# Kernel tuning notes

Measured on AMD Instinct MI355X. Metric: run time of the kernel, lower is better.

The kernel has to match this reference:

```python
import jax, jax.numpy as jnp
import numpy as np

DIM = 256; QK = 256; HEADS = 8; TOPK = 2; WV = 2; WH = 2
SCALE = QK ** -0.5


def setup_inputs() -> dict:
    key = jax.random.key(0)
    ks = jax.random.split(key, 6)
    x = jax.random.normal(ks[0], (4, DIM, 64, 64), jnp.float32)
    Wqkv = jax.random.normal(ks[1], (DIM, 2 * QK + DIM), jnp.float32) * 0.02
    bqkv = jnp.zeros((2 * QK + DIM,), jnp.float32)
    Wo = jax.random.normal(ks[2], (DIM, DIM), jnp.float32) * 0.02
    bo = jnp.zeros((DIM,), jnp.float32)
    lepe_w = jax.random.normal(ks[3], (3, 3, 1, DIM), jnp.float32) * 0.1  # HWIO depthwise
    lepe_b = jnp.zeros((DIM,), jnp.float32)
    return {"x": x, "Wqkv": Wqkv, "bqkv": bqkv, "Wo": Wo, "bo": bo,
            "lepe_w": lepe_w, "lepe_b": lepe_b}


def _dwconv(x, w, b):
    # depthwise 3x3 conv, NHWC
    y = jax.lax.conv_general_dilated(x, w, (1, 1), 'SAME',
                                     dimension_numbers=('NHWC', 'HWIO', 'NHWC'),
                                     feature_group_count=x.shape[-1])
    return y + b


def _branch(win, Wqkv, bqkv, lepe_w, lepe_b, to_image):
    n, p2, h, w, _ = win.shape
    w2 = h * w
    qkv = win @ Wqkv + bqkv
    q = qkv[..., :QK]
    kv = qkv[..., QK:]                                  # [n,p2,h,w,QK+DIM]
    q_pix = q.reshape(n, p2, w2, QK)
    kv_pix = kv.reshape(n, p2, w2, QK + DIM)            # identity kv_down
    # region routing (detached in original)
    q_win = jax.lax.stop_gradient(q).mean((2, 3))       # [n,p2,QK]
    k_win = jax.lax.stop_gradient(kv[..., :QK]).mean((2, 3))
    logit = jnp.einsum('npc,nqc->npq', q_win * SCALE, k_win)
    _, r_idx = jax.lax.top_k(logit, TOPK)               # [n,p2,TOPK]
    # gather selected KV windows (mul_weight='none')
    kv_sel = jax.vmap(lambda kvb, idxb: kvb[idxb])(kv_pix, r_idx)  # [n,p2,k,w2,ckv]
    k_sel = kv_sel[..., :QK].reshape(n, p2, TOPK * w2, HEADS, QK // HEADS)
    v_sel = kv_sel[..., QK:].reshape(n, p2, TOPK * w2, HEADS, DIM // HEADS)
    qh = q_pix.reshape(n, p2, w2, HEADS, QK // HEADS)
    attn = jax.nn.softmax(jnp.einsum('npqhd,npkhd->nphqk', qh * SCALE, k_sel), axis=-1)
    out = jnp.einsum('nphqk,npkhd->npqhd', attn, v_sel).reshape(n, p2, h, w, DIM)
    lepe = _dwconv(to_image(kv[..., QK:]), lepe_w, lepe_b)
    return to_image(out) + lepe


def reference(x, Wqkv, bqkv, Wo, bo, lepe_w, lepe_b):
    xh = x.transpose(0, 2, 3, 1)                        # NHWC
    N, H, W, C = xh.shape
    v_win, h_win = H // WV, W // WH
    # vertical branch: horizontal strips of height WV, full width
    vm = xh.reshape(N, v_win, WV, W, C)
    # horizontal branch: vertical strips of width WH, full height
    hm = xh.reshape(N, H, h_win, WH, C).transpose(0, 2, 1, 3, 4)
    img_v = lambda a: a.reshape(N, H, W, a.shape[-1])
    img_h = lambda a: a.transpose(0, 2, 1, 3, 4).reshape(N, H, W, a.shape[-1])
    o1 = _branch(vm, Wqkv, bqkv, lepe_w, lepe_b, img_v)
    o2 = _branch(hm, Wqkv, bqkv, lepe_w, lepe_b, img_h)
    out = (o1 @ Wo + bo) + (o2 @ Wo + bo)
    return out.transpose(0, 3, 1, 2)                    # back to NCHW
```

## Files before the change

kernel.cpp:

```cpp
#include <hip/hip_runtime.h>
#include <hip/hip_bf16.h>
#include <math.h>

#define NBATCH 4
#define HW     4096
#define NPIX   16384
#define SCALE  0.0625f
#define QLOG2E (0.0625f * 1.44269504088896340736f)

typedef __attribute__((ext_vector_type(8))) short bf16x8;
typedef __attribute__((ext_vector_type(4))) float f32x4;

__device__ __forceinline__ int pixmap(int b, int n, int p, int pos){
  return (b == 0) ? (n*HW + p*128 + pos)
                  : (n*HW + (pos >> 1)*64 + (p << 1) + (pos & 1));
}

__device__ __forceinline__ ushort f2b(float x){
  __hip_bfloat16 h = __float2bfloat16(x);
  return *reinterpret_cast<ushort*>(&h);
}
__device__ __forceinline__ float b2f(ushort u){
  __hip_bfloat16 h = *reinterpret_cast<__hip_bfloat16*>(&u);
  return __bfloat162float(h);
}
__device__ __forceinline__ uint pk2(float a, float b){
  return (uint)f2b(a) | ((uint)f2b(b) << 16);
}

__global__ __launch_bounds__(256) void k_xt(
    const float* __restrict__ x, ushort* __restrict__ Xb)
{
  __shared__ float T[32][257];
  const int n = blockIdx.y, hw0 = blockIdx.x * 32;
  const int tid = threadIdx.x;
  const int hl = tid & 31, cg = tid >> 5;
  #pragma unroll 8
  for(int i = 0; i < 32; i++){
    const int c = i*8 + cg;
    T[hl][c] = x[((size_t)(n*256 + c))*4096 + hw0 + hl];
  }
  __syncthreads();
  const int c0 = (tid & 31)*8, pb = tid >> 5;
  #pragma unroll
  for(int i = 0; i < 4; i++){
    const int p = pb + 8*i;
    union { bf16x8 v; ushort u[8]; } U;
    #pragma unroll
    for(int j = 0; j < 8; j++) U.u[j] = f2b(T[p][c0 + j]);
    *(bf16x8*)(Xb + ((size_t)(n*HW + hw0 + p))*256 + c0) = U.v;
  }
}

__global__ __launch_bounds__(256) void k_wt(
    const float* __restrict__ Wqkv, ushort* __restrict__ Wt)
{
  const int o = blockIdx.x, t = threadIdx.x;
  Wt[(size_t)o*256 + t] = f2b(Wqkv[(size_t)t*768 + o]);
}

__global__ __launch_bounds__(256) void k_wto(
    const float* __restrict__ Wo, ushort* __restrict__ WoT)
{
  const int o = blockIdx.x, t = threadIdx.x;
  WoT[(size_t)o*256 + t] = f2b(Wo[(size_t)t*256 + o]);
}

__global__ __launch_bounds__(256) void k_qkv_mfma(
    const ushort* __restrict__ Xb, const ushort* __restrict__ Wt,
    const float* __restrict__ bqkv, ushort* __restrict__ QKVb,
    ushort* __restrict__ Vt)
{
  const int tid = threadIdx.x;
  const int l = tid & 63, w = tid >> 6;
  const int wr = w >> 1, wc = w & 1;
  const int q16 = l & 15, g = l >> 4;
  const int row0 = blockIdx.x*128 + wr*64;
  const int col0 = blockIdx.y*128 + wc*64;

  f32x4 acc[4][4];
  #pragma unroll
  for(int i = 0; i < 4; i++)
    #pragma unroll
    for(int j = 0; j < 4; j++) acc[i][j] = (f32x4){0,0,0,0};

  const ushort* Ab = Xb + (size_t)(row0 + q16)*256 + 8*g;
  const ushort* Bb = Wt + (size_t)(col0 + q16)*256 + 8*g;

  #pragma unroll
  for(int ks = 0; ks < 8; ks++){
    const int k0 = ks*32;
    bf16x8 a[4], b[4];
    #pragma unroll
    for(int i = 0; i < 4; i++) a[i] = *(const bf16x8*)(Ab + (size_t)(16*i)*256 + k0);
    #pragma unroll
    for(int j = 0; j < 4; j++) b[j] = *(const bf16x8*)(Bb + (size_t)(16*j)*256 + k0);
    #pragma unroll
    for(int i = 0; i < 4; i++)
      #pragma unroll
      for(int j = 0; j < 4; j++)
        acc[i][j] = __builtin_amdgcn_mfma_f32_16x16x32_bf16(a[i], b[j], acc[i][j], 0, 0, 0);
  }

  const int n = row0 >> 12, hwb = row0 & 4095;
  #pragma unroll
  for(int j = 0; j < 4; j++){
    const int col = col0 + 16*j + q16;
    const float bias = bqkv[col];
    const float sc = (col < 256) ? QLOG2E : 1.f;
    #pragma unroll
    for(int i = 0; i < 4; i++){
      ushort4 u;
      u.x = f2b((acc[i][j][0] + bias) * sc);
      u.y = f2b((acc[i][j][1] + bias) * sc);
      u.z = f2b((acc[i][j][2] + bias) * sc);
      u.w = f2b((acc[i][j][3] + bias) * sc);
      const int row = row0 + 16*i + 4*g;
      QKVb[(size_t)(row+0)*768 + col] = u.x;
      QKVb[(size_t)(row+1)*768 + col] = u.y;
      QKVb[(size_t)(row+2)*768 + col] = u.z;
      QKVb[(size_t)(row+3)*768 + col] = u.w;
      if(col >= 512){
        *(ushort4*)&Vt[((size_t)(n*256 + col - 512))*4096 + hwb + 16*i + 4*g] = u;
      }
    }
  }
}

__global__ __launch_bounds__(256) void k_xmean(
    const float* __restrict__ x, float* __restrict__ xwin)
{
  const int n = blockIdx.y;
  const int c = blockIdx.x*4 + (threadIdx.x >> 6);
  const int l = threadIdx.x & 63;
  const float* xc = x + ((size_t)(n*256 + c))*4096;

  float4 cs[8];
  #pragma unroll
  for(int i = 0; i < 8; i++) cs[i] = (float4){0,0,0,0};
  float rsum = 0.f;
  const float4* xr = (const float4*)(xc + l*64);
  #pragma unroll
  for(int i = 0; i < 16; i++){
    const float4 v = xr[i];
    rsum += (v.x+v.y)+(v.z+v.w);
    const float p0 = v.x+v.y, p1 = v.z+v.w;
    if(i & 1){ cs[i>>1].z += p0; cs[i>>1].w += p1; }
    else     { cs[i>>1].x += p0; cs[i>>1].y += p1; }
  }
  #pragma unroll
  for(int i = 0; i < 8; i++){
    #pragma unroll
    for(int s = 1; s < 64; s <<= 1){
      cs[i].x += __shfl_xor(cs[i].x, s);
      cs[i].y += __shfl_xor(cs[i].y, s);
      cs[i].z += __shfl_xor(cs[i].z, s);
      cs[i].w += __shfl_xor(cs[i].w, s);
    }
  }
  const int p = l & 31;
  const float rp = __shfl(rsum, 2*p) + __shfl(rsum, 2*p + 1);
  float cp;
  {
    const int hi = p >> 2, lo = p & 3;
    const float4 q = hi==0?cs[0]:hi==1?cs[1]:hi==2?cs[2]:hi==3?cs[3]
                   : hi==4?cs[4]:hi==5?cs[5]:hi==6?cs[6]:cs[7];
    cp = lo==0?q.x : lo==1?q.y : lo==2?q.z : q.w;
  }
  if(l < 32){
    xwin[((size_t)((0*NBATCH + n)*32 + p))*256 + c] = rp * (1.f/128.f);
    xwin[((size_t)((1*NBATCH + n)*32 + p))*256 + c] = cp * (1.f/128.f);
  }
}

__global__ __launch_bounds__(256) void k_win_gemm(
    const float* __restrict__ xwin, const float* __restrict__ Wqkv,
    const float* __restrict__ bqkv, float* __restrict__ qwin, float* __restrict__ kwin)
{
  __shared__ float xs[256];
  const int row = blockIdx.x;
  const int tid = threadIdx.x;
  xs[tid] = xwin[(size_t)row*256 + tid];
  __syncthreads();
  #pragma unroll
  for(int half = 0; half < 2; half++){
    const int col = half*256 + tid;
    float s = 0.f;
    for(int k = 0; k < 256; k++) s += xs[k] * Wqkv[(size_t)k*768 + col];
    s += bqkv[col];
    if(half == 0) qwin[(size_t)row*256 + tid] = s;
    else          kwin[(size_t)row*256 + tid] = s;
  }
}

__global__ __launch_bounds__(256) void k_logits_top2(
    const float* __restrict__ qwin, const float* __restrict__ kwin, int* __restrict__ ridx)
{
  const int n = blockIdx.x, b = blockIdx.y;
  __shared__ float lg[32][32];
  const int base = ((b*NBATCH + n)*32)*256;
  for(int t = threadIdx.x; t < 1024; t += 256){
    const int p = t >> 5, q = t & 31;
    const float* qp = qwin + base + p*256;
    const float* kq = kwin + base + q*256;
    float s = 0.f;
    for(int c = 0; c < 256; c++) s += qp[c]*kq[c];
    lg[p][q] = s * SCALE;
  }
  __syncthreads();
  if(threadIdx.x < 32){
    const int p = threadIdx.x;
    float m0 = -INFINITY; int i0 = 0;
    for(int q = 0; q < 32; q++){ const float v = lg[p][q]; if(v > m0){ m0 = v; i0 = q; } }
    float m1 = -INFINITY; int i1 = 0;
    for(int q = 0; q < 32; q++){ if(q == i0) continue; const float v = lg[p][q]; if(v > m1){ m1 = v; i1 = q; } }
    const int o = ((b*NBATCH + n)*32 + p)*2;
    ridx[o] = i0; ridx[o+1] = i1;
  }
}

__global__ __launch_bounds__(256) void k_attn_mfma(
    const ushort* __restrict__ QKVb, const ushort* __restrict__ Vt,
    const int* __restrict__ ridx, ushort* __restrict__ Ob)
{
  int id = blockIdx.x*4 + (threadIdx.x >> 6);
  const int half = id & 1; id >>= 1;
  const int hd = id & 7;  id >>= 3;
  const int p  = id & 31; id >>= 5;
  const int n  = id & 3;  id >>= 2;
  const int b  = id;
  const int l = threadIdx.x & 63;
  const int q16 = l & 15, g = l >> 4;

  const int ro = ((b*NBATCH + n)*32 + p)*2;
  const int r0 = ridx[ro], r1 = ridx[ro+1];

  int qpix[4];
  bf16x8 qf[4];
  #pragma unroll
  for(int m = 0; m < 4; m++){
    qpix[m] = pixmap(b, n, p, (half*4 + m)*16 + q16);
    qf[m] = *(const bf16x8*)(QKVb + (size_t)qpix[m]*768 + hd*32 + 8*g);
  }

  f32x4 acc0[4], acc1[4];
  float rs[4];
  #pragma unroll
  for(int m = 0; m < 4; m++){
    acc0[m] = (f32x4){0,0,0,0}; acc1[m] = (f32x4){0,0,0,0}; rs[m] = 0.f;
  }

  for(int c = 0; c < 8; c++){
    const int wsel = (c < 4) ? r0 : r1;
    const int posb = (32*c) & 127;

    bf16x8 kf0, kf1;
    {
      const int kp0 = pixmap(b, n, wsel, posb + q16);
      kf0 = *(const bf16x8*)(QKVb + (size_t)kp0*768 + 256 + hd*32 + 8*g);
      const int kp1 = pixmap(b, n, wsel, posb + 16 + q16);
      kf1 = *(const bf16x8*)(QKVb + (size_t)kp1*768 + 256 + hd*32 + 8*g);
    }
    bf16x8 vf0, vf1;
    if(b == 0){
      const ushort* base = Vt + ((size_t)(n*256 + hd*32 + q16))*4096 + wsel*128 + posb + 4*g;
      union { bf16x8 v; ushort4 h[2]; } U0, U1;
      U0.h[0] = *(const ushort4*)(base);
      U0.h[1] = *(const ushort4*)(base + 16);
      U1.h[0] = *(const ushort4*)(base + (size_t)16*4096);
      U1.h[1] = *(const ushort4*)(base + (size_t)16*4096 + 16);
      vf0 = U0.v; vf1 = U1.v;
    } else {
      const int h0 = (posb + 4*g) >> 1;
      const ushort* base = Vt + ((size_t)(n*256 + hd*32 + q16))*4096 + 2*wsel;
      union { bf16x8 v; uint u[4]; } U0, U1;
      U0.u[0] = *(const uint*)(base + (h0    )*64);
      U0.u[1] = *(const uint*)(base + (h0 + 1)*64);
      U0.u[2] = *(const uint*)(base + (h0 + 8)*64);
      U0.u[3] = *(const uint*)(base + (h0 + 9)*64);
      const ushort* base1 = base + (size_t)16*4096;
      U1.u[0] = *(const uint*)(base1 + (h0    )*64);
      U1.u[1] = *(const uint*)(base1 + (h0 + 1)*64);
      U1.u[2] = *(const uint*)(base1 + (h0 + 8)*64);
      U1.u[3] = *(const uint*)(base1 + (h0 + 9)*64);
      vf0 = U0.v; vf1 = U1.v;
    }

    #pragma unroll
    for(int m = 0; m < 4; m++){
      const f32x4 z = {0,0,0,0};
      f32x4 s0 = __builtin_amdgcn_mfma_f32_16x16x32_bf16(kf0, qf[m], z, 0, 0, 0);
      f32x4 s1 = __builtin_amdgcn_mfma_f32_16x16x32_bf16(kf1, qf[m], z, 0, 0, 0);
      const float e00 = exp2f(s0[0]), e01 = exp2f(s0[1]), e02 = exp2f(s0[2]), e03 = exp2f(s0[3]);
      const float e10 = exp2f(s1[0]), e11 = exp2f(s1[1]), e12 = exp2f(s1[2]), e13 = exp2f(s1[3]);
      rs[m] += ((e00+e01)+(e02+e03)) + ((e10+e11)+(e12+e13));
      union { bf16x8 v; uint u[4]; } P;
      P.u[0] = pk2(e00, e01);
      P.u[1] = pk2(e02, e03);
      P.u[2] = pk2(e10, e11);
      P.u[3] = pk2(e12, e13);
      acc0[m] = __builtin_amdgcn_mfma_f32_16x16x32_bf16(vf0, P.v, acc0[m], 0, 0, 0);
      acc1[m] = __builtin_amdgcn_mfma_f32_16x16x32_bf16(vf1, P.v, acc1[m], 0, 0, 0);
    }
  }

  #pragma unroll
  for(int m = 0; m < 4; m++){
    float r = rs[m];
    r += __shfl_xor(r, 16);
    r += __shfl_xor(r, 32);
    rs[m] = 1.f / r;
  }
  #pragma unroll
  for(int m = 0; m < 4; m++){
    ushort* op = Ob + ((size_t)b*NPIX + qpix[m])*256 + hd*32 + 4*g;
    const float iv = rs[m];
    ushort4 o0 = { f2b(acc0[m][0]*iv), f2b(acc0[m][1]*iv), f2b(acc0[m][2]*iv), f2b(acc0[m][3]*iv) };
    ushort4 o1 = { f2b(acc1[m][0]*iv), f2b(acc1[m][1]*iv), f2b(acc1[m][2]*iv), f2b(acc1[m][3]*iv) };
    *(ushort4*)op = o0;
    *(ushort4*)(op + 16) = o1;
  }
}

__global__ __launch_bounds__(256) void k_combine_lepe(
    const ushort* __restrict__ QKVb, const ushort* __restrict__ Ob0,
    const ushort* __restrict__ Ob1,
    const float* __restrict__ lw, const float* __restrict__ lb, ushort* __restrict__ Sb)
{
  const int pix = blockIdx.x;
  const int c = threadIdx.x;
  const int n = pix >> 12, rem = pix & 4095;
  const int h = rem >> 6, w = rem & 63;
  float conv = 0.f;
  #pragma unroll
  for(int kh = 0; kh < 3; kh++){
    const int hh = h + kh - 1;
    if(hh < 0 || hh >= 64) continue;
    #pragma unroll
    for(int kw = 0; kw < 3; kw++){
      const int wi = w + kw - 1;
      if(wi < 0 || wi >= 64) continue;
      const int np = (n*64 + hh)*64 + wi;
      conv += b2f(QKVb[(size_t)np*768 + 512 + c]) * lw[(kh*3 + kw)*256 + c];
    }
  }
  const size_t idx = (size_t)pix*256 + c;
  Sb[idx] = f2b(b2f(Ob0[idx]) + b2f(Ob1[idx]) + 2.f*(conv + lb[c]));
}

__global__ __launch_bounds__(256) void k_out_mfma(
    const ushort* __restrict__ Sb, const ushort* __restrict__ WoT,
    const float* __restrict__ bo, float* __restrict__ out)
{
  const int tid = threadIdx.x;
  const int l = tid & 63, w = tid >> 6;
  const int wr = w >> 1, wc = w & 1;
  const int q16 = l & 15, g = l >> 4;
  const int c0   = blockIdx.x*128 + wr*64;
  const int pix0 = blockIdx.y*128 + wc*64;
  const int n = pix0 >> 12, rem0 = pix0 & 4095;

  f32x4 acc[4][4];
  #pragma unroll
  for(int i = 0; i < 4; i++)
    #pragma unroll
    for(int j = 0; j < 4; j++) acc[i][j] = (f32x4){0,0,0,0};

  const ushort* Ab = WoT + (size_t)(c0 + q16)*256 + 8*g;
  const ushort* Bb = Sb  + (size_t)(pix0 + q16)*256 + 8*g;

  #pragma unroll
  for(int ks = 0; ks < 8; ks++){
    const int k0 = ks*32;
    bf16x8 a[4], b[4];
    #pragma unroll
    for(int i = 0; i < 4; i++) a[i] = *(const bf16x8*)(Ab + (size_t)(16*i)*256 + k0);
    #pragma unroll
    for(int j = 0; j < 4; j++) b[j] = *(const bf16x8*)(Bb + (size_t)(16*j)*256 + k0);
    #pragma unroll
    for(int i = 0; i < 4; i++)
      #pragma unroll
      for(int j = 0; j < 4; j++)
        acc[i][j] = __builtin_amdgcn_mfma_f32_16x16x32_bf16(a[i], b[j], acc[i][j], 0, 0, 0);
  }

  float* outn = out + (size_t)n*256*4096;
  #pragma unroll
  for(int i = 0; i < 4; i++){
    #pragma unroll
    for(int r = 0; r < 4; r++){
      const int c = c0 + 16*i + 4*g + r;
      const float bias = 2.f*bo[c];
      #pragma unroll
      for(int j = 0; j < 4; j++){
        const int rem = rem0 + 16*j + q16;
        outn[(size_t)c*4096 + rem] = acc[i][j][r] + bias;
      }
    }
  }
}

extern "C" void kernel_launch(void* const* d_in, const int* in_sizes, int n_in,
                              void* d_out, int out_size, void* d_ws, size_t ws_size,
                              hipStream_t stream)
{
  const float* x    = (const float*)d_in[0];
  const float* Wqkv = (const float*)d_in[1];
  const float* bqkv = (const float*)d_in[2];
  const float* Wo   = (const float*)d_in[3];
  const float* bo   = (const float*)d_in[4];
  const float* lw   = (const float*)d_in[5];
  const float* lb   = (const float*)d_in[6];
  float* out = (float*)d_out;

  char* w = (char*)d_ws;
  ushort* Xb   = (ushort*)w; w += (size_t)NPIX*256*2;
  ushort* Wt   = (ushort*)w; w += (size_t)768*256*2;
  ushort* WoT  = (ushort*)w; w += (size_t)256*256*2;
  ushort* QKVb = (ushort*)w; w += (size_t)NPIX*768*2;
  ushort* Vt   = (ushort*)w; w += (size_t)NPIX*256*2;
  ushort* Ob   = (ushort*)w; w += (size_t)2*NPIX*256*2;
  ushort* Sb   = (ushort*)w; w += (size_t)NPIX*256*2;
  float*  xwin = (float*)w;  w += (size_t)2*NBATCH*32*256*4;
  float*  qwin = (float*)w;  w += (size_t)2*NBATCH*32*256*4;
  float*  kwin = (float*)w;  w += (size_t)2*NBATCH*32*256*4;
  int*    ridx = (int*)w;    w += (size_t)2*NBATCH*32*2*4;

  ushort* Ob0 = Ob;
  ushort* Ob1 = Ob + (size_t)NPIX*256;

  k_xt          <<<dim3(128,NBATCH), 256, 0, stream>>>(x, Xb);
  k_wt          <<<768, 256, 0, stream>>>(Wqkv, Wt);
  k_wto         <<<256, 256, 0, stream>>>(Wo, WoT);
  k_qkv_mfma    <<<dim3(128,6), 256, 0, stream>>>(Xb, Wt, bqkv, QKVb, Vt);
  k_xmean       <<<dim3(64,NBATCH), 256, 0, stream>>>(x, xwin);
  k_win_gemm    <<<256, 256, 0, stream>>>(xwin, Wqkv, bqkv, qwin, kwin);
  k_logits_top2 <<<dim3(NBATCH,2), 256, 0, stream>>>(qwin, kwin, ridx);
  k_attn_mfma   <<<1024, 256, 0, stream>>>(QKVb, Vt, ridx, Ob);
  k_combine_lepe<<<NPIX, 256, 0, stream>>>(QKVb, Ob0, Ob1, lw, lb, Sb);
  k_out_mfma    <<<dim3(2,128), 256, 0, stream>>>(Sb, WoT, bo, out);
}
```

Measured before the change: 208.6 us.

## Process full window per wave and double-buffer KV fragment loads in attention

The attention kernel now has each wavefront handle all 128 query pixels of a window-head instead of half, so K/V fragments are loaded once and reused across eight query tiles. Launch blocks are halved to match. K/V loads are software-pipelined with two fragment buffers so the next chunk's global loads are issued before the current chunk's MFMA and exp work. This raises register pressure (8 query fragments, 16 accumulators) and halves the number of waves, which may reduce occupancy and latency hiding.

```diff
diff --git a/kernel.cpp b/kernel.cpp
--- a/kernel.cpp
+++ b/kernel.cpp
@@ -151,7 +151,8 @@
   #pragma unroll
   for(int i = 0; i < 8; i++){
     #pragma unroll
-    for(int s = 1; s < 64; s <<= 1){
+    for(int sb = 0; sb < 6; sb++){
+      const int s = 1 << sb;
       cs[i].x += __shfl_xor(cs[i].x, s);
       cs[i].y += __shfl_xor(cs[i].y, s);
       cs[i].z += __shfl_xor(cs[i].z, s);
@@ -219,12 +220,48 @@
   }
 }
 
+struct KVFrag { bf16x8 kf0, kf1, vf0, vf1; };
+
+__device__ __forceinline__ KVFrag load_kv(
+    const ushort* __restrict__ QKVb, const ushort* __restrict__ Vt,
+    int b, int n, int wsel, int posb, int hd, int q16, int g)
+{
+  KVFrag f;
+  const int kp0 = pixmap(b, n, wsel, posb + q16);
+  f.kf0 = *(const bf16x8*)(QKVb + (size_t)kp0*768 + 256 + hd*32 + 8*g);
+  const int kp1 = pixmap(b, n, wsel, posb + 16 + q16);
+  f.kf1 = *(const bf16x8*)(QKVb + (size_t)kp1*768 + 256 + hd*32 + 8*g);
+  if(b == 0){
+    const ushort* base = Vt + ((size_t)(n*256 + hd*32 + q16))*4096 + wsel*128 + posb + 4*g;
+    union { bf16x8 v; ushort4 h[2]; } U0, U1;
+    U0.h[0] = *(const ushort4*)(base);
+    U0.h[1] = *(const ushort4*)(base + 16);
+    U1.h[0] = *(const ushort4*)(base + (size_t)16*4096);
+    U1.h[1] = *(const ushort4*)(base + (size_t)16*4096 + 16);
+    f.vf0 = U0.v; f.vf1 = U1.v;
+  } else {
+    const int h0 = (posb + 4*g) >> 1;
+    const ushort* base = Vt + ((size_t)(n*256 + hd*32 + q16))*4096 + 2*wsel;
+    union { bf16x8 v; uint u[4]; } U0, U1;
+    U0.u[0] = *(const uint*)(base + (h0    )*64);
+    U0.u[1] = *(const uint*)(base + (h0 + 1)*64);
+    U0.u[2] = *(const uint*)(base + (h0 + 8)*64);
+    U0.u[3] = *(const uint*)(base + (h0 + 9)*64);
+    const ushort* base1 = base + (size_t)16*4096;
+    U1.u[0] = *(const uint*)(base1 + (h0    )*64);
+    U1.u[1] = *(const uint*)(base1 + (h0 + 1)*64);
+    U1.u[2] = *(const uint*)(base1 + (h0 + 8)*64);
+    U1.u[3] = *(const uint*)(base1 + (h0 + 9)*64);
+    f.vf0 = U0.v; f.vf1 = U1.v;
+  }
+  return f;
+}
+
 __global__ __launch_bounds__(256) void k_attn_mfma(
     const ushort* __restrict__ QKVb, const ushort* __restrict__ Vt,
     const int* __restrict__ ridx, ushort* __restrict__ Ob)
 {
   int id = blockIdx.x*4 + (threadIdx.x >> 6);
-  const int half = id & 1; id >>= 1;
   const int hd = id & 7;  id >>= 3;
   const int p  = id & 31; id >>= 5;
   const int n  = id & 3;  id >>= 2;
@@ -235,84 +272,61 @@
   const int ro = ((b*NBATCH + n)*32 + p)*2;
   const int r0 = ridx[ro], r1 = ridx[ro+1];
 
-  int qpix[4];
-  bf16x8 qf[4];
-  #pragma unroll
-  for(int m = 0; m < 4; m++){
-    qpix[m] = pixmap(b, n, p, (half*4 + m)*16 + q16);
+  int qpix[8];
+  bf16x8 qf[8];
+  #pragma unroll
+  for(int m = 0; m < 8; m++){
+    qpix[m] = pixmap(b, n, p, m*16 + q16);
     qf[m] = *(const bf16x8*)(QKVb + (size_t)qpix[m]*768 + hd*32 + 8*g);
   }
 
-  f32x4 acc0[4], acc1[4];
-  float rs[4];
-  #pragma unroll
-  for(int m = 0; m < 4; m++){
+  f32x4 acc0[8], acc1[8];
+  float rs[8];
+  #pragma unroll
+  for(int m = 0; m < 8; m++){
     acc0[m] = (f32x4){0,0,0,0}; acc1[m] = (f32x4){0,0,0,0}; rs[m] = 0.f;
   }
 
-  for(int c = 0; c < 8; c++){
-    const int wsel = (c < 4) ? r0 : r1;
-    const int posb = (32*c) & 127;
-
-    bf16x8 kf0, kf1;
-    {
-      const int kp0 = pixmap(b, n, wsel, posb + q16);
-      kf0 = *(const bf16x8*)(QKVb + (size_t)kp0*768 + 256 + hd*32 + 8*g);
-      const int kp1 = pixmap(b, n, wsel, posb + 16 + q16);
-      kf1 = *(const bf16x8*)(QKVb + (size_t)kp1*768 + 256 + hd*32 + 8*g);
-    }
-    bf16x8 vf0, vf1;
-    if(b == 0){
-      const ushort* base = Vt + ((size_t)(n*256 + hd*32 + q16))*4096 + wsel*128 + posb + 4*g;
-      union { bf16x8 v; ushort4 h[2]; } U0, U1;
-      U0.h[0] = *(const ushort4*)(base);
-      U0.h[1] = *(const ushort4*)(base + 16);
-      U1.h[0] = *(const ushort4*)(base + (size_t)16*4096);
-      U1.h[1] = *(const ushort4*)(base + (size_t)16*4096 + 16);
-      vf0 = U0.v; vf1 = U1.v;
-    } else {
-      const int h0 = (posb + 4*g) >> 1;
-      const ushort* base = Vt + ((size_t)(n*256 + hd*32 + q16))*4096 + 2*wsel;
-      union { bf16x8 v; uint u[4]; } U0, U1;
-      U0.u[0] = *(const uint*)(base + (h0    )*64);
-      U0.u[1] = *(const uint*)(base + (h0 + 1)*64);
-      U0.u[2] = *(const uint*)(base + (h0 + 8)*64);
-      U0.u[3] = *(const uint*)(base + (h0 + 9)*64);
-      const ushort* base1 = base + (size_t)16*4096;
-      U1.u[0] = *(const uint*)(base1 + (h0    )*64);
-      U1.u[1] = *(const uint*)(base1 + (h0 + 1)*64);
-      U1.u[2] = *(const uint*)(base1 + (h0 + 8)*64);
-      U1.u[3] = *(const uint*)(base1 + (h0 + 9)*64);
-      vf0 = U0.v; vf1 = U1.v;
-    }
-
-    #pragma unroll
-    for(int m = 0; m < 4; m++){
-      const f32x4 z = {0,0,0,0};
-      f32x4 s0 = __builtin_amdgcn_mfma_f32_16x16x32_bf16(kf0, qf[m], z, 0, 0, 0);
-      f32x4 s1 = __builtin_amdgcn_mfma_f32_16x16x32_bf16(kf1, qf[m], z, 0, 0, 0);
-      const float e00 = exp2f(s0[0]), e01 = exp2f(s0[1]), e02 = exp2f(s0[2]), e03 = exp2f(s0[3]);
-      const float e10 = exp2f(s1[0]), e11 = exp2f(s1[1]), e12 = exp2f(s1[2]), e13 = exp2f(s1[3]);
-      rs[m] += ((e00+e01)+(e02+e03)) + ((e10+e11)+(e12+e13));
-      union { bf16x8 v; uint u[4]; } P;
-      P.u[0] = pk2(e00, e01);
-      P.u[1] = pk2(e02, e03);
-      P.u[2] = pk2(e10, e11);
-      P.u[3] = pk2(e12, e13);
-      acc0[m] = __builtin_amdgcn_mfma_f32_16x16x32_bf16(vf0, P.v, acc0[m], 0, 0, 0);
-      acc1[m] = __builtin_amdgcn_mfma_f32_16x16x32_bf16(vf1, P.v, acc1[m], 0, 0, 0);
-    }
-  }
-
-  #pragma unroll
-  for(int m = 0; m < 4; m++){
+  #define COMPUTE(F)                                                            \
+    _Pragma("unroll")                                                           \
+    for(int m = 0; m < 8; m++){                                                 \
+      const f32x4 z = {0,0,0,0};                                                \
+      f32x4 s0 = __builtin_amdgcn_mfma_f32_16x16x32_bf16((F).kf0, qf[m], z, 0, 0, 0); \
+      f32x4 s1 = __builtin_amdgcn_mfma_f32_16x16x32_bf16((F).kf1, qf[m], z, 0, 0, 0); \
+      const float e00 = exp2f(s0[0]), e01 = exp2f(s0[1]), e02 = exp2f(s0[2]), e03 = exp2f(s0[3]); \
+      const float e10 = exp2f(s1[0]), e11 = exp2f(s1[1]), e12 = exp2f(s1[2]), e13 = exp2f(s1[3]); \
+      rs[m] += ((e00+e01)+(e02+e03)) + ((e10+e11)+(e12+e13));                   \
+      union { bf16x8 v; uint u[4]; } P;                                         \
+      P.u[0] = pk2(e00, e01);                                                   \
+      P.u[1] = pk2(e02, e03);                                                   \
+      P.u[2] = pk2(e10, e11);                                                   \
+      P.u[3] = pk2(e12, e13);                                                   \
+      acc0[m] = __builtin_amdgcn_mfma_f32_16x16x32_bf16((F).vf0, P.v, acc0[m], 0, 0, 0); \
+      acc1[m] = __builtin_amdgcn_mfma_f32_16x16x32_bf16((F).vf1, P.v, acc1[m], 0, 0, 0); \
+    }
+
+  KVFrag fA = load_kv(QKVb, Vt, b, n, r0, 0, hd, q16, g);
+  for(int cc = 0; cc < 8; cc += 2){
+    const int w1 = (cc+1 < 4) ? r0 : r1;
+    KVFrag fB = load_kv(QKVb, Vt, b, n, w1, (32*(cc+1)) & 127, hd, q16, g);
+    COMPUTE(fA);
+    if(cc + 2 < 8){
+      const int w2 = (cc+2 < 4) ? r0 : r1;
+      fA = load_kv(QKVb, Vt, b, n, w2, (32*(cc+2)) & 127, hd, q16, g);
+    }
+    COMPUTE(fB);
+  }
+  #undef COMPUTE
+
+  #pragma unroll
+  for(int m = 0; m < 8; m++){
     float r = rs[m];
     r += __shfl_xor(r, 16);
     r += __shfl_xor(r, 32);
     rs[m] = 1.f / r;
   }
   #pragma unroll
-  for(int m = 0; m < 4; m++){
+  for(int m = 0; m < 8; m++){
     ushort* op = Ob + ((size_t)b*NPIX + qpix[m])*256 + hd*32 + 4*g;
     const float iv = rs[m];
     ushort4 o0 = { f2b(acc0[m][0]*iv), f2b(acc0[m][1]*iv), f2b(acc0[m][2]*iv), f2b(acc0[m][3]*iv) };
@@ -436,7 +450,7 @@
   k_xmean       <<<dim3(64,NBATCH), 256, 0, stream>>>(x, xwin);
   k_win_gemm    <<<256, 256, 0, stream>>>(xwin, Wqkv, bqkv, qwin, kwin);
   k_logits_top2 <<<dim3(NBATCH,2), 256, 0, stream>>>(qwin, kwin, ridx);
-  k_attn_mfma   <<<1024, 256, 0, stream>>>(QKVb, Vt, ridx, Ob);
+  k_attn_mfma   <<<512, 256, 0, stream>>>(QKVb, Vt, ridx, Ob);
   k_combine_lepe<<<NPIX, 256, 0, stream>>>(QKVb, Ob0, Ob1, lw, lb, Sb);
   k_out_mfma    <<<dim3(2,128), 256, 0, stream>>>(Sb, WoT, bo, out);
 }
```

Result: faster. 186.3 us (-10.7%).
